# Kernel optimization log

Measured on AMD Instinct MI355X. Metric: run time of the kernel, lower is better.

## Reference

```python
import jax, jax.numpy as jnp
import numpy as np

N = 1024      # number of atoms
L = 64        # latent_size
VOCAB = 20    # vocab_size (len(ATOM_CATEGORIES))


def _lin(key, fan_in, fan_out):
    # mimic torch nn.Linear init: U(-1/sqrt(fan_in), 1/sqrt(fan_in))
    kw, kb = jax.random.split(key)
    s = 1.0 / np.sqrt(fan_in)
    W = jax.random.uniform(kw, (fan_in, fan_out), minval=-s, maxval=s, dtype=jnp.float32)
    b = jax.random.uniform(kb, (fan_out,), minval=-s, maxval=s, dtype=jnp.float32)
    return W, b


def setup_inputs() -> dict:
    key = jax.random.key(0)
    ks = jax.random.split(key, 9)
    We1, be1 = _lin(ks[3], 2 * L + 1, L)   # mlp_e layer 1
    We2, be2 = _lin(ks[4], L, L)           # mlp_e layer 2
    Wh1, bh1 = _lin(ks[5], L + 1, L)       # mlp_h layer 1
    Wh2, bh2 = _lin(ks[6], L, L)           # mlp_h layer 2
    Wo, bo = _lin(ks[7], L, 1)             # output_mlp
    return {
        "atom_categories": jax.random.randint(ks[0], (N,), 0, VOCAB),
        "atom_coordinates": jax.random.normal(ks[1], (N, 3), dtype=jnp.float32),
        "learnable_matrix": jax.random.normal(ks[2], (VOCAB, L), dtype=jnp.float32),
        "We1": We1, "be1": be1, "We2": We2, "be2": be2,
        "Wh1": Wh1, "bh1": bh1, "Wh2": Wh2, "bh2": bh2,
        "Wo": Wo, "bo": bo,
    }


def reference(atom_categories, atom_coordinates, learnable_matrix,
              We1, be1, We2, be2, Wh1, bh1, Wh2, bh2, Wo, bo):
    Z = atom_coordinates
    # init_H: learnable_matrix.T @ one_hot(cat) == row gather
    H = learnable_matrix[atom_categories]                       # [N, L]

    # pairwise squared distances ||Z_i - Z_j||^2
    d2 = jnp.sum((Z[:, None, :] - Z[None, :, :]) ** 2, axis=-1)  # [N, N]

    # mlp_e layer 1 on concat(H_i, H_j, d2): split We1 to avoid materializing concat
    W1i, W1j, w1z = We1[:L], We1[L:2 * L], We1[2 * L]            # [L,L],[L,L],[L]
    pre_i = H @ W1i                                              # [N, L]
    pre_j = H @ W1j                                              # [N, L]
    h1 = jnp.tanh(pre_i[:, None, :] + pre_j[None, :, :]
                  + d2[:, :, None] * w1z + be1)                  # [N, N, L]
    W_e = jnp.tanh(h1 @ We2 + be2)                               # [N, N, L]

    # V[i] = sum over j != i of sum_l W_e[i,j,l]
    total = jnp.sum(W_e, axis=(1, 2))                            # [N]
    diag = jnp.einsum('iil->i', W_e)                             # [N]
    V = total - diag                                             # [N]

    # mlp_h on concat(H_i, V_i): split Wh1
    hh = jnp.tanh(H @ Wh1[:L] + V[:, None] * Wh1[L] + bh1)       # [N, L]
    newH = jnp.tanh(hh @ Wh2 + bh2)                              # [N, L]

    Hsum = jnp.sum(newH, axis=0)                                 # [L]
    return (Hsum @ Wo + bo)[0]                                   # scalar
```

## Files before the change

kernel.cpp:

```cpp
#include <hip/hip_runtime.h>
#include <hip/hip_bf16.h>


#define N_ATOMS 1024
#define L_DIM 64
#define TPB 256
#define CSCALE 2.8853900817779268f

typedef _Float16 f16x8 __attribute__((ext_vector_type(8)));
typedef __fp16  fp16x2 __attribute__((ext_vector_type(2)));
typedef float f32x4 __attribute__((ext_vector_type(4)));

__device__ __forceinline__ float tanh_fast(float x) {
    float e = __builtin_amdgcn_exp2f(x * CSCALE);
    float r = __builtin_amdgcn_rcpf(e + 1.0f);
    return fmaf(-2.0f, r, 1.0f);
}

__global__ __launch_bounds__(256) void k_prep(const int* __restrict__ cat,
                                              const float* __restrict__ LM,
                                              const float* __restrict__ We1,
                                              const float* __restrict__ be1,
                                              float* __restrict__ H,
                                              float* __restrict__ preI,
                                              float* __restrict__ P3,
                                              float* __restrict__ out) {
    int t = threadIdx.x;
    int sub = t >> 6, l = t & 63;
    int i = blockIdx.x * 4 + sub;
    if (blockIdx.x == 0 && t == 0) out[0] = 0.f;
    __shared__ float hrow[4][L_DIM];
    float hv = LM[cat[i] * L_DIM + l];
    hrow[sub][l] = hv;
    H[i * L_DIM + l] = hv;
    __syncthreads();
    float s1 = 0.f, s2 = 0.f;
#pragma unroll
    for (int m = 0; m < L_DIM; m++) {
        float h = hrow[sub][m];
        s1 = fmaf(h, We1[m * L_DIM + l], s1);
        s2 = fmaf(h, We1[(L_DIM + m) * L_DIM + l], s2);
    }
    preI[i * L_DIM + l] = s1 * CSCALE;
    int cc = i >> 4;
    int Ll = i & 15;
    int quad = (l >> 3) & 3;
    int L = quad * 16 + Ll;
    int g = ((l >> 5) << 1) | ((l >> 2) & 1);
    int e2 = l & 3;
    P3[cc * 1024 + g * 256 + L * 4 + e2] = (s2 + be1[l]) * CSCALE;
}

__global__ __launch_bounds__(TPB) void k_main(const float* __restrict__ Z,
                                              const float* __restrict__ We1,
                                              const float* __restrict__ We2,
                                              const float* __restrict__ be2,
                                              const float* __restrict__ preI,
                                              const float* __restrict__ P3,
                                              const float* __restrict__ H,
                                              const float* __restrict__ Wh1,
                                              const float* __restrict__ bh1,
                                              const float* __restrict__ Wh2,
                                              const float* __restrict__ bh2,
                                              const float* __restrict__ Wo,
                                              const float* __restrict__ bo,
                                              float* __restrict__ out) {
    int i = blockIdx.x;
    int t = threadIdx.x;
    int lane = t & 63;
    int wave = t >> 6;
    int nlo = lane & 15;
    int quad = lane >> 4;

    __shared__ float d2s[N_ATOMS];
    __shared__ float red[TPB];
    __shared__ float hrow_s[L_DIM];
    __shared__ float hh_s[L_DIM];
    __shared__ float dgt[L_DIM];
    __shared__ f16x8 bLs[8 * 64];

    float zi0 = Z[i * 3], zi1 = Z[i * 3 + 1], zi2 = Z[i * 3 + 2];
    for (int p = t; p < N_ATOMS; p += TPB) {
        float a = zi0 - Z[p * 3], b = zi1 - Z[p * 3 + 1], c = zi2 - Z[p * 3 + 2];
        d2s[p] = a * a + b * b + c * c;
    }

    f32x4 aiR[4], wzR[4];
#pragma unroll
    for (int g = 0; g < 4; g++) {
        int mb = ((g >> 1) << 5) + (quad << 3) + ((g & 1) << 2);
        aiR[g] = *(const f32x4*)(preI + i * L_DIM + mb);
        f32x4 wz = *(const f32x4*)(We1 + 2 * L_DIM * L_DIM + mb);
        wzR[g] = wz * CSCALE;
    }

    f16x8 bH[4][2];
    float biasR[4];
#pragma unroll
    for (int nt = 0; nt < 4; nt++) {
        float psum = 0.f;
#pragma unroll
        for (int kt = 0; kt < 2; kt++) {
            f16x8 hi8, lo8;
#pragma unroll
            for (int e = 0; e < 8; e++) {
                float x = We2[(kt * 32 + quad * 8 + e) * L_DIM + nt * 16 + nlo];
                psum += x;
                float wp = -2.0f * CSCALE * x;
                _Float16 hi = (_Float16)wp;
                hi8[e] = hi;
                lo8[e] = (_Float16)(wp - (float)hi);
            }
            bH[nt][kt] = hi8;
            if (wave == 0) bLs[(kt * 4 + nt) * 64 + lane] = lo8;
        }
        psum += __shfl_xor(psum, 16);
        psum += __shfl_xor(psum, 32);
        biasR[nt] = CSCALE * (be2[nt * 16 + nlo] + psum);
    }

    const float* Pbase = P3 + wave * 16 * 1024 + lane * 4;
    f32x4 p0 = *(const f32x4*)(Pbase + 0 * 256);
    f32x4 p1 = *(const f32x4*)(Pbase + 1 * 256);
    f32x4 p2 = *(const f32x4*)(Pbase + 2 * 256);
    f32x4 p3 = *(const f32x4*)(Pbase + 3 * 256);

    __syncthreads();

    float Vr = 0.f;
    for (int k = 0; k < 16; k++) {
        int j0 = (wave * 16 + k) * 16;
        float d2 = d2s[j0 + nlo];

        float h[4][4];
#pragma unroll
        for (int e2 = 0; e2 < 4; e2++) {
            {
                float z = fmaf(d2, wzR[0][e2], aiR[0][e2] + p0[e2]);
                h[0][e2] = __builtin_amdgcn_rcpf(__builtin_amdgcn_exp2f(z) + 1.0f);
            }
            {
                float z = fmaf(d2, wzR[1][e2], aiR[1][e2] + p1[e2]);
                h[1][e2] = __builtin_amdgcn_rcpf(__builtin_amdgcn_exp2f(z) + 1.0f);
            }
            {
                float z = fmaf(d2, wzR[2][e2], aiR[2][e2] + p2[e2]);
                h[2][e2] = __builtin_amdgcn_rcpf(__builtin_amdgcn_exp2f(z) + 1.0f);
            }
            {
                float z = fmaf(d2, wzR[3][e2], aiR[3][e2] + p3[e2]);
                h[3][e2] = __builtin_amdgcn_rcpf(__builtin_amdgcn_exp2f(z) + 1.0f);
            }
        }
        union { f16x8 v; fp16x2 h2[4]; } u0, u1;
        u0.h2[0] = __builtin_amdgcn_cvt_pkrtz(h[0][0], h[0][1]);
        u0.h2[1] = __builtin_amdgcn_cvt_pkrtz(h[0][2], h[0][3]);
        u0.h2[2] = __builtin_amdgcn_cvt_pkrtz(h[1][0], h[1][1]);
        u0.h2[3] = __builtin_amdgcn_cvt_pkrtz(h[1][2], h[1][3]);
        u1.h2[0] = __builtin_amdgcn_cvt_pkrtz(h[2][0], h[2][1]);
        u1.h2[1] = __builtin_amdgcn_cvt_pkrtz(h[2][2], h[2][3]);
        u1.h2[2] = __builtin_amdgcn_cvt_pkrtz(h[3][0], h[3][1]);
        u1.h2[3] = __builtin_amdgcn_cvt_pkrtz(h[3][2], h[3][3]);
        f16x8 aH0 = u0.v, aH1 = u1.v;

        if (k < 15) {
            const float* nb = Pbase + (k + 1) * 1024;
            p0 = *(const f32x4*)(nb + 0 * 256);
            p1 = *(const f32x4*)(nb + 1 * 256);
            p2 = *(const f32x4*)(nb + 2 * 256);
            p3 = *(const f32x4*)(nb + 3 * 256);
        }

#pragma unroll
        for (int nt = 0; nt < 4; nt++) {
            f16x8 bl0 = bLs[(0 * 4 + nt) * 64 + lane];
            f16x8 bl1 = bLs[(1 * 4 + nt) * 64 + lane];
            f32x4 acc = {biasR[nt], biasR[nt], biasR[nt], biasR[nt]};
            acc = __builtin_amdgcn_mfma_f32_16x16x32_f16(aH0, bH[nt][0], acc, 0, 0, 0);
            acc = __builtin_amdgcn_mfma_f32_16x16x32_f16(aH0, bl0, acc, 0, 0, 0);
            acc = __builtin_amdgcn_mfma_f32_16x16x32_f16(aH1, bH[nt][1], acc, 0, 0, 0);
            acc = __builtin_amdgcn_mfma_f32_16x16x32_f16(aH1, bl1, acc, 0, 0, 0);
#pragma unroll
            for (int r4 = 0; r4 < 4; r4++) {
                float e = __builtin_amdgcn_exp2f(acc[r4]);
                Vr += __builtin_amdgcn_rcpf(e + 1.0f);
            }
        }
    }

    red[t] = Vr;
    __syncthreads();

    float Rall;
    if (t < 64) {
        float r = red[t] + red[t + 64] + red[t + 128] + red[t + 192];
#pragma unroll
        for (int o = 32; o > 0; o >>= 1) r += __shfl_xor(r, o);
        Rall = r;
        int cc = i >> 4, Ll = i & 15;
        int q2 = (t >> 3) & 3;
        int g = ((t >> 5) << 1) | ((t >> 2) & 1);
        float z = preI[i * L_DIM + t] + P3[cc * 1024 + g * 256 + (q2 * 16 + Ll) * 4 + (t & 3)];
        float rr = __builtin_amdgcn_rcpf(__builtin_amdgcn_exp2f(z) + 1.0f);
        dgt[t] = fmaf(-2.0f, rr, 1.0f);
        hrow_s[t] = H[i * L_DIM + t];
    }
    __syncthreads();
    if (t < 64) {
        float S = be2[t];
#pragma unroll
        for (int m = 0; m < L_DIM; m++) S = fmaf(dgt[m], We2[m * L_DIM + t], S);
        float rd = __builtin_amdgcn_rcpf(__builtin_amdgcn_exp2f(S * CSCALE) + 1.0f);
#pragma unroll
        for (int o = 32; o > 0; o >>= 1) rd += __shfl_xor(rd, o);
        float V = fmaf(-2.0f, Rall - rd, (float)(1023 * L_DIM));
        float s = 0.f;
#pragma unroll
        for (int m = 0; m < L_DIM; m++) s = fmaf(hrow_s[m], Wh1[m * L_DIM + t], s);
        s = fmaf(V, Wh1[L_DIM * L_DIM + t], s) + bh1[t];
        hh_s[t] = tanh_fast(s);
    }
    __syncthreads();
    if (t < 64) {
        float s2 = 0.f;
#pragma unroll
        for (int m = 0; m < L_DIM; m++) s2 = fmaf(hh_s[m], Wh2[m * L_DIM + t], s2);
        float nh = tanh_fast(s2 + bh2[t]);
        float w = nh * Wo[t];
#pragma unroll
        for (int o = 32; o > 0; o >>= 1) w += __shfl_down(w, o);
        if (t == 0) atomicAdd(out, w + (i == 0 ? bo[0] : 0.f));
    }
}

extern "C" void kernel_launch(void* const* d_in, const int* in_sizes, int n_in,
                              void* d_out, int out_size, void* d_ws, size_t ws_size,
                              hipStream_t stream) {
    const int*   cat = (const int*)  d_in[0];
    const float* Z   = (const float*)d_in[1];
    const float* LM  = (const float*)d_in[2];
    const float* We1 = (const float*)d_in[3];
    const float* be1 = (const float*)d_in[4];
    const float* We2 = (const float*)d_in[5];
    const float* be2 = (const float*)d_in[6];
    const float* Wh1 = (const float*)d_in[7];
    const float* bh1 = (const float*)d_in[8];
    const float* Wh2 = (const float*)d_in[9];
    const float* bh2 = (const float*)d_in[10];
    const float* Wo  = (const float*)d_in[11];
    const float* bo  = (const float*)d_in[12];
    float* out = (float*)d_out;

    float* ws   = (float*)d_ws;
    float* H    = ws;
    float* preI = H    + N_ATOMS * L_DIM;
    float* P3   = preI + N_ATOMS * L_DIM;

    k_prep<<<N_ATOMS / 4, 256, 0, stream>>>(cat, LM, We1, be1, H, preI, P3, out);
    k_main<<<N_ATOMS, TPB, 0, stream>>>(Z, We1, We2, be2, preI, P3, H,
                                        Wh1, bh1, Wh2, bh2, Wo, bo, out);
}
```

Measured before the change: 122.8 us.

## Split pairwise loop across eight waves per block and use packed vector math

Raises the block size from 256 to 512 threads, so each of 8 waves handles 8 column tiles of j instead of 4 waves handling 16. The final per-wave reduction now sums 8 partials. It also folds the aiR bias into the prefetched P3 values and rewrites the first-layer pre-activation and the sigmoid accumulation as f32x4 vector ops, so the compiler can emit packed FMA and add instructions. The goal is shorter per-block serial loops, better latency hiding and fewer VALU instructions. The cost is more per-wave setup of the B fragments, higher register and LDS pressure per block, and reliance on the red buffer and launch bounds supporting 512 threads.

New measurement: 142.5 us. 1.16x slower.

```diff
diff --git a/kernel.cpp b/kernel.cpp
--- a/kernel.cpp
+++ b/kernel.cpp
@@ -4,7 +4,7 @@
 
 #define N_ATOMS 1024
 #define L_DIM 64
-#define TPB 256
+#define TPB 512
 #define CSCALE 2.8853900817779268f
 
 typedef _Float16 f16x8 __attribute__((ext_vector_type(8)));
@@ -119,56 +119,58 @@
         biasR[nt] = CSCALE * (be2[nt * 16 + nlo] + psum);
     }
 
-    const float* Pbase = P3 + wave * 16 * 1024 + lane * 4;
-    f32x4 p0 = *(const f32x4*)(Pbase + 0 * 256);
-    f32x4 p1 = *(const f32x4*)(Pbase + 1 * 256);
-    f32x4 p2 = *(const f32x4*)(Pbase + 2 * 256);
-    f32x4 p3 = *(const f32x4*)(Pbase + 3 * 256);
-
-    __syncthreads();
-
-    float Vr = 0.f;
-    for (int k = 0; k < 16; k++) {
-        int j0 = (wave * 16 + k) * 16;
+    const float* Pbase = P3 + (wave * 8) * 1024 + lane * 4;
+    f32x4 p0 = *(const f32x4*)(Pbase + 0 * 256) + aiR[0];
+    f32x4 p1 = *(const f32x4*)(Pbase + 1 * 256) + aiR[1];
+    f32x4 p2 = *(const f32x4*)(Pbase + 2 * 256) + aiR[2];
+    f32x4 p3 = *(const f32x4*)(Pbase + 3 * 256) + aiR[3];
+
+    __syncthreads();
+
+    f32x4 Vr4 = {0.f, 0.f, 0.f, 0.f};
+    for (int k = 0; k < 8; k++) {
+        int j0 = (wave * 8 + k) * 16;
         float d2 = d2s[j0 + nlo];
-
-        float h[4][4];
-#pragma unroll
-        for (int e2 = 0; e2 < 4; e2++) {
-            {
-                float z = fmaf(d2, wzR[0][e2], aiR[0][e2] + p0[e2]);
-                h[0][e2] = __builtin_amdgcn_rcpf(__builtin_amdgcn_exp2f(z) + 1.0f);
-            }
-            {
-                float z = fmaf(d2, wzR[1][e2], aiR[1][e2] + p1[e2]);
-                h[1][e2] = __builtin_amdgcn_rcpf(__builtin_amdgcn_exp2f(z) + 1.0f);
-            }
-            {
-                float z = fmaf(d2, wzR[2][e2], aiR[2][e2] + p2[e2]);
-                h[2][e2] = __builtin_amdgcn_rcpf(__builtin_amdgcn_exp2f(z) + 1.0f);
-            }
-            {
-                float z = fmaf(d2, wzR[3][e2], aiR[3][e2] + p3[e2]);
-                h[3][e2] = __builtin_amdgcn_rcpf(__builtin_amdgcn_exp2f(z) + 1.0f);
-            }
+        f32x4 d2v = {d2, d2, d2, d2};
+
+        f32x4 z0 = p0 + d2v * wzR[0];
+        f32x4 z1 = p1 + d2v * wzR[1];
+        f32x4 z2 = p2 + d2v * wzR[2];
+        f32x4 z3 = p3 + d2v * wzR[3];
+        f32x4 ex0, ex1, ex2, ex3;
+#pragma unroll
+        for (int e = 0; e < 4; e++) {
+            ex0[e] = __builtin_amdgcn_exp2f(z0[e]);
+            ex1[e] = __builtin_amdgcn_exp2f(z1[e]);
+            ex2[e] = __builtin_amdgcn_exp2f(z2[e]);
+            ex3[e] = __builtin_amdgcn_exp2f(z3[e]);
+        }
+        ex0 += 1.0f; ex1 += 1.0f; ex2 += 1.0f; ex3 += 1.0f;
+        f32x4 r0, r1, r2, r3;
+#pragma unroll
+        for (int e = 0; e < 4; e++) {
+            r0[e] = __builtin_amdgcn_rcpf(ex0[e]);
+            r1[e] = __builtin_amdgcn_rcpf(ex1[e]);
+            r2[e] = __builtin_amdgcn_rcpf(ex2[e]);
+            r3[e] = __builtin_amdgcn_rcpf(ex3[e]);
         }
         union { f16x8 v; fp16x2 h2[4]; } u0, u1;
-        u0.h2[0] = __builtin_amdgcn_cvt_pkrtz(h[0][0], h[0][1]);
-        u0.h2[1] = __builtin_amdgcn_cvt_pkrtz(h[0][2], h[0][3]);
-        u0.h2[2] = __builtin_amdgcn_cvt_pkrtz(h[1][0], h[1][1]);
-        u0.h2[3] = __builtin_amdgcn_cvt_pkrtz(h[1][2], h[1][3]);
-        u1.h2[0] = __builtin_amdgcn_cvt_pkrtz(h[2][0], h[2][1]);
-        u1.h2[1] = __builtin_amdgcn_cvt_pkrtz(h[2][2], h[2][3]);
-        u1.h2[2] = __builtin_amdgcn_cvt_pkrtz(h[3][0], h[3][1]);
-        u1.h2[3] = __builtin_amdgcn_cvt_pkrtz(h[3][2], h[3][3]);
+        u0.h2[0] = __builtin_amdgcn_cvt_pkrtz(r0[0], r0[1]);
+        u0.h2[1] = __builtin_amdgcn_cvt_pkrtz(r0[2], r0[3]);
+        u0.h2[2] = __builtin_amdgcn_cvt_pkrtz(r1[0], r1[1]);
+        u0.h2[3] = __builtin_amdgcn_cvt_pkrtz(r1[2], r1[3]);
+        u1.h2[0] = __builtin_amdgcn_cvt_pkrtz(r2[0], r2[1]);
+        u1.h2[1] = __builtin_amdgcn_cvt_pkrtz(r2[2], r2[3]);
+        u1.h2[2] = __builtin_amdgcn_cvt_pkrtz(r3[0], r3[1]);
+        u1.h2[3] = __builtin_amdgcn_cvt_pkrtz(r3[2], r3[3]);
         f16x8 aH0 = u0.v, aH1 = u1.v;
 
-        if (k < 15) {
+        if (k < 7) {
             const float* nb = Pbase + (k + 1) * 1024;
-            p0 = *(const f32x4*)(nb + 0 * 256);
-            p1 = *(const f32x4*)(nb + 1 * 256);
-            p2 = *(const f32x4*)(nb + 2 * 256);
-            p3 = *(const f32x4*)(nb + 3 * 256);
+            p0 = *(const f32x4*)(nb + 0 * 256) + aiR[0];
+            p1 = *(const f32x4*)(nb + 1 * 256) + aiR[1];
+            p2 = *(const f32x4*)(nb + 2 * 256) + aiR[2];
+            p3 = *(const f32x4*)(nb + 3 * 256) + aiR[3];
         }
 
 #pragma unroll
@@ -180,20 +182,25 @@
             acc = __builtin_amdgcn_mfma_f32_16x16x32_f16(aH0, bl0, acc, 0, 0, 0);
             acc = __builtin_amdgcn_mfma_f32_16x16x32_f16(aH1, bH[nt][1], acc, 0, 0, 0);
             acc = __builtin_amdgcn_mfma_f32_16x16x32_f16(aH1, bl1, acc, 0, 0, 0);
-#pragma unroll
-            for (int r4 = 0; r4 < 4; r4++) {
-                float e = __builtin_amdgcn_exp2f(acc[r4]);
-                Vr += __builtin_amdgcn_rcpf(e + 1.0f);
-            }
-        }
-    }
-
-    red[t] = Vr;
+            f32x4 ev;
+#pragma unroll
+            for (int r4 = 0; r4 < 4; r4++) ev[r4] = __builtin_amdgcn_exp2f(acc[r4]);
+            ev += 1.0f;
+            f32x4 rv;
+#pragma unroll
+            for (int r4 = 0; r4 < 4; r4++) rv[r4] = __builtin_amdgcn_rcpf(ev[r4]);
+            Vr4 += rv;
+        }
+    }
+
+    red[t] = Vr4[0] + Vr4[1] + Vr4[2] + Vr4[3];
     __syncthreads();
 
     float Rall;
     if (t < 64) {
-        float r = red[t] + red[t + 64] + red[t + 128] + red[t + 192];
+        float r = red[t];
+#pragma unroll
+        for (int w = 1; w < 8; w++) r += red[t + 64 * w];
 #pragma unroll
         for (int o = 32; o > 0; o >>= 1) r += __shfl_xor(r, o);
         Rall = r;
```
